# Kernel tuning notes

Measured on AMD Instinct MI355X. Metric: run time of the kernel, lower is better.

## Reference

```python
import jax, jax.numpy as jnp
import numpy as np

B, N, C, H, NRES = 32, 1024, 384, 1024, 20
NTAB = 21  # 20 aa + unknown, per AlphaFold residue_constants


def setup_inputs() -> dict:
    key = jax.random.key(0)
    ks = jax.random.split(key, 16)
    s = 0.02
    inp = {}
    inp['act'] = jax.random.normal(ks[0], (B, N, C), jnp.float32)
    inp['angles'] = jax.random.normal(ks[1], (B, N, 7, 2), jnp.float32)
    inp['rigids'] = jax.random.normal(ks[2], (B, N, 7), jnp.float32)
    inp['fixed_mask'] = jax.random.randint(ks[3], (B, N), 0, 2, jnp.int32)
    inp['seq_t'] = jax.random.randint(ks[4], (B, N), 0, NRES, jnp.int32)
    inp['residx_atom37_to_atom14'] = jax.random.randint(ks[5], (B, N, 37), 0, 14, jnp.int32)
    inp['ln_g'] = jnp.ones((C,), jnp.float32)
    inp['ln_b'] = jnp.zeros((C,), jnp.float32)
    inp['w1'] = jax.random.normal(ks[6], (C, H), jnp.float32) * s
    inp['b1'] = jnp.zeros((H,), jnp.float32)
    inp['w2'] = jax.random.normal(ks[7], (H, H), jnp.float32) * s
    inp['b2'] = jnp.zeros((H,), jnp.float32)
    inp['w3'] = jax.random.normal(ks[8], (H, NRES), jnp.float32) * s
    inp['b3'] = jnp.zeros((NRES,), jnp.float32)
    # stand-in residue_constants tables (same shapes/dtypes as AlphaFold's)
    inp['default_frames'] = jax.random.normal(ks[9], (NTAB, 8, 4, 4), jnp.float32)
    inp['group_idx'] = jax.random.randint(ks[10], (NTAB, 14), 0, 8, jnp.int32)
    inp['atom14_mask'] = (jax.random.uniform(ks[11], (NTAB, 14)) > 0.3).astype(jnp.float32)
    inp['atom37_mask'] = (jax.random.uniform(ks[12], (NTAB, 37)) > 0.3).astype(jnp.float32)
    inp['lit_positions'] = jax.random.normal(ks[13], (NTAB, 14, 3), jnp.float32)
    return inp


def quat_to_rot(q):
    q = q / jnp.sqrt(jnp.sum(q * q, axis=-1, keepdims=True) + 1e-8)
    w, x, y, z = q[..., 0], q[..., 1], q[..., 2], q[..., 3]
    r = jnp.stack([
        1 - 2 * (y * y + z * z), 2 * (x * y - w * z), 2 * (x * z + w * y),
        2 * (x * y + w * z), 1 - 2 * (x * x + z * z), 2 * (y * z - w * x),
        2 * (x * z - w * y), 2 * (y * z + w * x), 1 - 2 * (x * x + y * y)
    ], axis=-1)
    return r.reshape(q.shape[:-1] + (3, 3))


def compose(r1, t1, r2, t2):
    # rigid composition: (r1, t1) o (r2, t2)
    return (jnp.einsum('...ij,...jk->...ik', r1, r2),
            jnp.einsum('...ij,...j->...i', r1, t2) + t1)


def reference(act, angles, rigids, fixed_mask, seq_t, residx_atom37_to_atom14,
              ln_g, ln_b, w1, b1, w2, b2, w3, b3,
              default_frames, group_idx, atom14_mask, atom37_mask, lit_positions):
    # --- small MLP head ---
    mu = jnp.mean(act, axis=-1, keepdims=True)
    var = jnp.var(act, axis=-1, keepdims=True)
    h = (act - mu) / jnp.sqrt(var + 1e-5) * ln_g + ln_b
    h = jax.nn.relu(h @ w1 + b1)
    h = jax.nn.relu(h @ w2 + b2)
    logits = h @ w3 + b3                                # [B,N,20]
    p_0t = jax.nn.softmax(logits, axis=-1)
    seq0 = jnp.argmax(p_0t, axis=-1).astype(jnp.int32)
    seq0 = seq0 * (1 - fixed_mask) + seq_t * fixed_mask  # [B,N]

    # --- backbone frame from quaternion rigids ---
    rb = quat_to_rot(rigids[..., :4])                    # [B,N,3,3]
    tb = rigids[..., 4:]                                 # [B,N,3]

    # --- torsion_angles_to_frames ---
    df = default_frames[seq0]                            # [B,N,8,4,4]
    dr, dt = df[..., :3, :3], df[..., :3, 3]
    sin, cos = angles[..., 0], angles[..., 1]            # [B,N,7]
    z1 = jnp.zeros_like(sin[..., :1])
    sin8 = jnp.concatenate([z1, sin], axis=-1)           # backbone group has angle 0
    cos8 = jnp.concatenate([jnp.ones_like(z1), cos], axis=-1)
    zz, oo = jnp.zeros_like(sin8), jnp.ones_like(sin8)
    rx = jnp.stack([oo, zz, zz, zz, cos8, -sin8, zz, sin8, cos8], axis=-1)
    rx = rx.reshape(sin8.shape + (3, 3))                 # rotation about x-axis
    fr = jnp.einsum('bngij,bngjk->bngik', dr, rx)        # frames to backbone (pre-chain)
    ft = dt
    # chain chi2->chi1, chi3->chi2, chi4->chi3
    r5, t5 = compose(fr[..., 4, :, :], ft[..., 4, :], fr[..., 5, :, :], ft[..., 5, :])
    r6, t6 = compose(r5, t5, fr[..., 6, :, :], ft[..., 6, :])
    r7, t7 = compose(r6, t6, fr[..., 7, :, :], ft[..., 7, :])
    frot = jnp.concatenate([fr[..., :5, :, :], r5[..., None, :, :], r6[..., None, :, :], r7[..., None, :, :]], axis=-3)
    ftr = jnp.concatenate([ft[..., :5, :], t5[..., None, :], t6[..., None, :], t7[..., None, :]], axis=-2)
    grot, gtr = compose(rb[..., None, :, :], tb[..., None, :], frot, ftr)  # [B,N,8,3,3],[B,N,8,3]

    # --- frames_and_literature_positions_to_atom14_pos ---
    gi = group_idx[seq0]                                 # [B,N,14]
    ar = jnp.take_along_axis(grot, jnp.broadcast_to(gi[..., None, None], gi.shape + (3, 3)), axis=2)
    at = jnp.take_along_axis(gtr, jnp.broadcast_to(gi[..., None], gi.shape + (3,)), axis=2)
    lit = lit_positions[seq0]                            # [B,N,14,3]
    m14 = atom14_mask[seq0]                              # [B,N,14]
    pred = (jnp.einsum('bnaij,bnaj->bnai', ar, lit) + at) * m14[..., None]

    # --- atom14 -> atom37 gather ---
    idx = residx_atom37_to_atom14
    final = jnp.take_along_axis(pred, jnp.broadcast_to(idx[..., None], idx.shape + (3,)), axis=2)
    m37 = atom37_mask[seq0]                              # [B,N,37]
    return logits, seq0, pred, final, m14, m37
```

## Files before the change

kernel.cpp:

```cpp
#include <hip/hip_runtime.h>
#include <math.h>

#define B_ 32
#define N_ 1024
#define C_ 384
#define H_ 1024
#define NRES 20
#define NTAB 21
#define M_TOTAL (B_*N_)
#define BK 32

typedef __attribute__((ext_vector_type(8))) short bf16x8;
typedef __attribute__((ext_vector_type(4))) float f32x4;

#define GLOAD_LDS(gptr, lptr) \
    __builtin_amdgcn_global_load_lds( \
        (const __attribute__((address_space(1))) void*)(gptr), \
        (__attribute__((address_space(3))) void*)(lptr), 16, 0, 0)

__device__ inline short bf16_rne(float v) {
    unsigned u = __float_as_uint(v);
    unsigned r = u + 0x7fffu + ((u >> 16) & 1u);
    return (short)(r >> 16);
}
__device__ inline void split2(float v, short& h, short& l) {
    unsigned u = __float_as_uint(v);
    unsigned r = (u + 0x7fffu + ((u >> 16) & 1u)) & 0xffff0000u;
    h = (short)(r >> 16);
    l = bf16_rne(v - __uint_as_float(r));
}

__global__ __launch_bounds__(256) void ln_split_kernel(const float* __restrict__ act,
                                                       const float* __restrict__ lng,
                                                       const float* __restrict__ lnb,
                                                       short* __restrict__ Xh,
                                                       short* __restrict__ Xl) {
    int wave = threadIdx.x >> 6;
    int lane = threadIdx.x & 63;
    int row  = blockIdx.x * 4 + wave;
    const float* x = act + (size_t)row * C_;
    float v[6];
    float s = 0.f;
#pragma unroll
    for (int i = 0; i < 6; i++) { v[i] = x[lane + i*64]; s += v[i]; }
#pragma unroll
    for (int off = 32; off > 0; off >>= 1) s += __shfl_xor(s, off, 64);
    float mu = s * (1.0f/384.0f);
    float vs = 0.f;
#pragma unroll
    for (int i = 0; i < 6; i++) { float d = v[i]-mu; vs += d*d; }
#pragma unroll
    for (int off = 32; off > 0; off >>= 1) vs += __shfl_xor(vs, off, 64);
    float rstd = 1.0f / sqrtf(vs * (1.0f/384.0f) + 1e-5f);
#pragma unroll
    for (int i = 0; i < 6; i++) {
        int col = lane + i*64;
        float y = (v[i] - mu) * rstd * lng[col] + lnb[col];
        short h, l; split2(y, h, l);
        Xh[(size_t)row * C_ + col] = h;
        Xl[(size_t)row * C_ + col] = l;
    }
}

__global__ __launch_bounds__(256) void conv_w_kernel(const float* __restrict__ w,
                                                     short* __restrict__ th,
                                                     short* __restrict__ tl,
                                                     int K, int N, int Npad) {
    __shared__ float t[32][33];
    int n0 = blockIdx.x * 32, k0 = blockIdx.y * 32;
    int tx = threadIdx.x & 31, ty = threadIdx.x >> 5;
#pragma unroll
    for (int i = ty; i < 32; i += 8) {
        int k = k0 + i, n = n0 + tx;
        t[i][tx] = (n < N) ? w[(size_t)k * N + n] : 0.f;
    }
    __syncthreads();
#pragma unroll
    for (int i = ty; i < 32; i += 8) {
        int n = n0 + i, k = k0 + tx;
        short h, l; split2(t[tx][i], h, l);
        th[(size_t)n * K + k] = h;
        tl[(size_t)n * K + k] = l;
    }
}

__global__ __launch_bounds__(512, 2) void presplit_gemm256(
    const short* __restrict__ Ahg, const short* __restrict__ Alg,
    const short* __restrict__ BTh, const short* __restrict__ BTl,
    const float* __restrict__ bias,
    short* __restrict__ Ch, short* __restrict__ Cl,
    int K, int ldc)
{
    __shared__ short P[4][2][256][32];
    const int BUFS = 256*32;
    int tid = threadIdx.x;
    int m0 = blockIdx.x * 256;
    int n0 = blockIdx.y * 256;
    int lane = tid & 63, wv = tid >> 6;
    int wr = wv >> 2, wc = wv & 3;
    int fm = lane & 15, kg = lane >> 4;

    int pl = wv >> 1, hf = wv & 1;
    const short* gsrc = (pl == 0) ? Ahg : (pl == 1) ? Alg : (pl == 2) ? BTh : BTl;
    int base = (pl < 2) ? m0 : n0;
    int swcb = (lane & 3) ^ ((lane >> 3) & 3);
    const short* gp = gsrc + (size_t)(base + hf*128 + (lane >> 2)) * K + swcb * 8;
    short* lpl = &P[pl][0][0][0] + hf * (128*32);

    int sz = (kg ^ ((fm >> 1) & 3)) * 8;
    const short* raH = &P[0][0][wr*128 + fm][0] + sz;
    const short* raL = &P[1][0][wr*128 + fm][0] + sz;
    const short* rbH = &P[2][0][wc*64  + fm][0] + sz;
    const short* rbL = &P[3][0][wc*64  + fm][0] + sz;

#define STAGE8(bsel, koff) \
    { _Pragma("unroll") \
      for (int c = 0; c < 8; c++) \
          GLOAD_LDS(gp + (size_t)(c*16) * K + (koff), lpl + (bsel)*BUFS + c*512); }

#define TRIPLE(ai, aj, AH, AL, BH, BL) { \
    f32x4 cc = acc[ai][aj]; \
    cc = __builtin_amdgcn_mfma_f32_16x16x32_bf16(AL, BH, cc, 0, 0, 0); \
    cc = __builtin_amdgcn_mfma_f32_16x16x32_bf16(AH, BL, cc, 0, 0, 0); \
    cc = __builtin_amdgcn_mfma_f32_16x16x32_bf16(AH, BH, cc, 0, 0, 0); \
    acc[ai][aj] = cc; }

    f32x4 acc[8][4] = {};
    const int NT = K / BK;

    bf16x8 aAh[4], aAl[4], aBh[4], aBl[4];
    bf16x8 bAh[2], bAl[2], bBh[2], bBl[2];

    STAGE8(0, 0);
    asm volatile("s_waitcnt vmcnt(0)" ::: "memory");
    __builtin_amdgcn_s_barrier();
#pragma unroll
    for (int i = 0; i < 4; i++) {
        aAh[i] = *(const bf16x8*)(raH + i*512);
        aAl[i] = *(const bf16x8*)(raL + i*512);
    }

    for (int t = 0; t < NT; ++t) {
        int cur = t & 1, nxt = cur ^ 1;
        size_t koff = (size_t)(t + 1) * BK;
        bool pf = (t + 1 < NT);

#pragma unroll
        for (int j = 0; j < 2; j++) {
            bAh[j] = *(const bf16x8*)(rbH + cur*BUFS + j*512);
            bAl[j] = *(const bf16x8*)(rbL + cur*BUFS + j*512);
            bBh[j] = *(const bf16x8*)(rbH + cur*BUFS + (2+j)*512);
            bBl[j] = *(const bf16x8*)(rbL + cur*BUFS + (2+j)*512);
        }
        if (pf) STAGE8(nxt, koff);
        __builtin_amdgcn_s_setprio(1);
#pragma unroll
        for (int i = 0; i < 4; i++)
#pragma unroll
            for (int j = 0; j < 2; j++) TRIPLE(i, j, aAh[i], aAl[i], bAh[j], bAl[j]);
        __builtin_amdgcn_s_setprio(0);
        __builtin_amdgcn_s_barrier();

#pragma unroll
        for (int i = 0; i < 4; i++) {
            aBh[i] = *(const bf16x8*)(raH + cur*BUFS + (4+i)*512);
            aBl[i] = *(const bf16x8*)(raL + cur*BUFS + (4+i)*512);
        }
        __builtin_amdgcn_s_setprio(1);
#pragma unroll
        for (int i = 0; i < 4; i++)
#pragma unroll
            for (int j = 0; j < 2; j++) TRIPLE(i, 2+j, aAh[i], aAl[i], bBh[j], bBl[j]);
        __builtin_amdgcn_s_setprio(0);
        __builtin_amdgcn_s_barrier();

        __builtin_amdgcn_s_setprio(1);
#pragma unroll
        for (int i = 0; i < 4; i++)
#pragma unroll
            for (int j = 0; j < 2; j++) TRIPLE(4+i, 2+j, aBh[i], aBl[i], bBh[j], bBl[j]);
        __builtin_amdgcn_s_setprio(0);
        asm volatile("s_waitcnt vmcnt(0)" ::: "memory");
        __builtin_amdgcn_s_barrier();

        if (pf) {
#pragma unroll
            for (int i = 0; i < 4; i++) {
                aAh[i] = *(const bf16x8*)(raH + nxt*BUFS + i*512);
                aAl[i] = *(const bf16x8*)(raL + nxt*BUFS + i*512);
            }
        }
        __builtin_amdgcn_s_setprio(1);
#pragma unroll
        for (int i = 0; i < 4; i++)
#pragma unroll
            for (int j = 0; j < 2; j++) TRIPLE(4+i, j, aBh[i], aBl[i], bAh[j], bAl[j]);
        __builtin_amdgcn_s_setprio(0);
        __builtin_amdgcn_s_barrier();
    }

#pragma unroll
    for (int i = 0; i < 8; i++)
#pragma unroll
        for (int j = 0; j < 4; j++) {
            int col = n0 + wc*64 + j*16 + fm;
            float bs = bias[col];
#pragma unroll
            for (int r = 0; r < 4; r++) {
                int row = m0 + wr*128 + i*16 + kg*4 + r;
                float v = fmaxf(acc[i][j][r] + bs, 0.f);
                short h, l; split2(v, h, l);
                Ch[(size_t)row * ldc + col] = h;
                Cl[(size_t)row * ldc + col] = l;
            }
        }
#undef STAGE8
#undef TRIPLE
}

__global__ __launch_bounds__(256) void gemm3_fused(
    const short* __restrict__ Ahg, const short* __restrict__ Alg,
    const short* __restrict__ BTh, const short* __restrict__ BTl,
    const float* __restrict__ b3,
    const int* __restrict__ fixed_mask, const int* __restrict__ seq_t,
    float* __restrict__ out_logits, float* __restrict__ seq_out,
    int* __restrict__ seq_int, int m0c)
{
    __shared__ short Ah[2][64][32], Al[2][64][32];
    __shared__ short Bh[2][32][32], Bl[2][32][32];
    __shared__ float slog[64][33];
    int tid = threadIdx.x;
    int m0 = blockIdx.x * 64;
    int lane = tid & 63, wv = tid >> 6;
    int wm = wv * 16;
    int fm = lane & 15, kg = lane >> 4;

    const short* gsrc = (wv == 0) ? Ahg : (wv == 1) ? Alg : (wv == 2) ? BTh : BTl;
    short* lb0 = (wv == 0) ? &Ah[0][0][0] : (wv == 1) ? &Al[0][0][0]
               : (wv == 2) ? &Bh[0][0][0] : &Bl[0][0][0];
    int pstride = (wv < 2) ? (64*32) : (32*32);
    int ncalls  = (wv < 2) ? 4 : 2;
    int base = (wv < 2) ? m0 : 0;
    int swcb = (lane & 3) ^ ((lane >> 3) & 3);
    const short* gp = gsrc + (size_t)(base + (lane >> 2)) * H_ + swcb * 8;

    int saz = (kg ^ (((wm + fm) >> 1) & 3)) * 8;
    int sbz[2];
#pragma unroll
    for (int j = 0; j < 2; j++) sbz[j] = (kg ^ (((j*16 + fm) >> 1) & 3)) * 8;

    f32x4 acc[2] = {};
    const int NT = H_ / BK;

    for (int c = 0; c < ncalls; c++)
        GLOAD_LDS(gp + (size_t)(c * 16) * H_, lb0 + c * 512);

    for (int t = 0; t < NT; ++t) {
        __syncthreads();

        if (t + 1 < NT) {
            short* lb = lb0 + ((t + 1) & 1) * pstride;
            size_t k0n = (size_t)(t + 1) * BK;
            for (int c = 0; c < ncalls; c++)
                GLOAD_LDS(gp + (size_t)(c * 16) * H_ + k0n, lb + c * 512);
        }

        int cur = t & 1;
        bf16x8 a_h = *(bf16x8*)&Ah[cur][wm + fm][saz];
        bf16x8 a_l = *(bf16x8*)&Al[cur][wm + fm][saz];
        bf16x8 b_h[2], b_l[2];
#pragma unroll
        for (int j = 0; j < 2; j++) {
            b_h[j] = *(bf16x8*)&Bh[cur][j*16 + fm][sbz[j]];
            b_l[j] = *(bf16x8*)&Bl[cur][j*16 + fm][sbz[j]];
        }
#pragma unroll
        for (int j = 0; j < 2; j++) {
            f32x4 c = acc[j];
            c = __builtin_amdgcn_mfma_f32_16x16x32_bf16(a_l, b_h[j], c, 0, 0, 0);
            c = __builtin_amdgcn_mfma_f32_16x16x32_bf16(a_h, b_l[j], c, 0, 0, 0);
            c = __builtin_amdgcn_mfma_f32_16x16x32_bf16(a_h, b_h[j], c, 0, 0, 0);
            acc[j] = c;
        }
    }

#pragma unroll
    for (int j = 0; j < 2; j++)
#pragma unroll
        for (int r = 0; r < 4; r++)
            slog[wm + kg*4 + r][j*16 + fm] = acc[j][r];
    __syncthreads();

    if (tid < 64) {
        int grow = m0c + m0 + tid;
        float best = -1e30f; int bi = 0;
        float* lg = out_logits + (size_t)grow * NRES;
#pragma unroll
        for (int n = 0; n < NRES; n++) {
            float s = slog[tid][n] + b3[n];
            lg[n] = s;
            if (s > best) { best = s; bi = n; }
        }
        int fmk = fixed_mask[grow];
        int s = fmk ? seq_t[grow] : bi;
        seq_int[grow] = s;
        seq_out[grow] = (float)s;
    }
}

__global__ __launch_bounds__(128) void geom_kernel(
    const float* __restrict__ angles, const float* __restrict__ rigids,
    const int* __restrict__ seq0i, const int* __restrict__ residx,
    const float* __restrict__ dframes, const int* __restrict__ gidx,
    const float* __restrict__ a14m, const float* __restrict__ a37m,
    const float* __restrict__ litp,
    float* __restrict__ out_pred, float* __restrict__ out_final,
    float* __restrict__ out_m14, float* __restrict__ out_m37)
{
    __shared__ float sdf[NTAB*8*16];
    __shared__ int   sgi[NTAB*14];
    __shared__ float sm14[NTAB*14];
    __shared__ float sm37[NTAB*37];
    __shared__ float slit[NTAB*14*3];
    __shared__ float predL[128][43];

    for (int i = threadIdx.x; i < NTAB*128; i += 128) sdf[i] = dframes[i];
    for (int i = threadIdx.x; i < NTAB*14; i += 128) { sgi[i] = gidx[i]; sm14[i] = a14m[i]; }
    for (int i = threadIdx.x; i < NTAB*37; i += 128) sm37[i] = a37m[i];
    for (int i = threadIdx.x; i < NTAB*42; i += 128) slit[i] = litp[i];
    __syncthreads();

    int p = blockIdx.x * 128 + threadIdx.x;
    int s = seq0i[p];

    const float* rg = rigids + (size_t)p * 7;
    float qw = rg[0], qx = rg[1], qy = rg[2], qz = rg[3];
    float tbx = rg[4], tby = rg[5], tbz = rg[6];
    float qn = 1.0f / sqrtf(qw*qw + qx*qx + qy*qy + qz*qz + 1e-8f);
    qw *= qn; qx *= qn; qy *= qn; qz *= qn;
    float rb[9];
    rb[0] = 1.f - 2.f*(qy*qy + qz*qz); rb[1] = 2.f*(qx*qy - qw*qz); rb[2] = 2.f*(qx*qz + qw*qy);
    rb[3] = 2.f*(qx*qy + qw*qz); rb[4] = 1.f - 2.f*(qx*qx + qz*qz); rb[5] = 2.f*(qy*qz - qw*qx);
    rb[6] = 2.f*(qx*qz - qw*qy); rb[7] = 2.f*(qy*qz + qw*qx); rb[8] = 1.f - 2.f*(qx*qx + qy*qy);

    float fr[8][9], ft[8][3];
    const float* ang = angles + (size_t)p * 14;
#pragma unroll
    for (int g = 0; g < 8; g++) {
        const float* df = &sdf[(s*8 + g)*16];
        float c, sn;
        if (g == 0) { c = 1.f; sn = 0.f; }
        else { sn = ang[(g-1)*2 + 0]; c = ang[(g-1)*2 + 1]; }
#pragma unroll
        for (int i = 0; i < 3; i++) {
            float d0 = df[i*4+0], d1 = df[i*4+1], d2 = df[i*4+2];
            fr[g][i*3+0] = d0;
            fr[g][i*3+1] = d1*c + d2*sn;
            fr[g][i*3+2] = d2*c - d1*sn;
            ft[g][i] = df[i*4+3];
        }
    }
#pragma unroll
    for (int g = 5; g <= 7; g++) {
        float r[9], t[3];
        const float* r1 = fr[g-1];
        const float* t1 = ft[g-1];
#pragma unroll
        for (int i = 0; i < 3; i++) {
#pragma unroll
            for (int j = 0; j < 3; j++)
                r[i*3+j] = r1[i*3+0]*fr[g][0*3+j] + r1[i*3+1]*fr[g][1*3+j] + r1[i*3+2]*fr[g][2*3+j];
            t[i] = r1[i*3+0]*ft[g][0] + r1[i*3+1]*ft[g][1] + r1[i*3+2]*ft[g][2] + t1[i];
        }
#pragma unroll
        for (int i = 0; i < 9; i++) fr[g][i] = r[i];
#pragma unroll
        for (int i = 0; i < 3; i++) ft[g][i] = t[i];
    }
#pragma unroll
    for (int g = 0; g < 8; g++) {
        float r[9], t[3];
#pragma unroll
        for (int i = 0; i < 3; i++) {
#pragma unroll
            for (int j = 0; j < 3; j++)
                r[i*3+j] = rb[i*3+0]*fr[g][0*3+j] + rb[i*3+1]*fr[g][1*3+j] + rb[i*3+2]*fr[g][2*3+j];
            t[i] = rb[i*3+0]*ft[g][0] + rb[i*3+1]*ft[g][1] + rb[i*3+2]*ft[g][2];
        }
#pragma unroll
        for (int i = 0; i < 9; i++) fr[g][i] = r[i];
        ft[g][0]=t[0]+tbx; ft[g][1]=t[1]+tby; ft[g][2]=t[2]+tbz;
    }
#pragma unroll
    for (int g = 0; g < 8; g++) {
#pragma unroll
        for (int a = 0; a < 14; a++) {
            if (sgi[s*14 + a] == g) {
                float m  = sm14[s*14 + a];
                float lx = slit[(s*14 + a)*3 + 0];
                float ly = slit[(s*14 + a)*3 + 1];
                float lz = slit[(s*14 + a)*3 + 2];
                float px = (fr[g][0]*lx + fr[g][1]*ly + fr[g][2]*lz + ft[g][0]) * m;
                float py = (fr[g][3]*lx + fr[g][4]*ly + fr[g][5]*lz + ft[g][1]) * m;
                float pz = (fr[g][6]*lx + fr[g][7]*ly + fr[g][8]*lz + ft[g][2]) * m;
                predL[threadIdx.x][a*3+0] = px;
                predL[threadIdx.x][a*3+1] = py;
                predL[threadIdx.x][a*3+2] = pz;
                out_pred[((size_t)p*14 + a)*3 + 0] = px;
                out_pred[((size_t)p*14 + a)*3 + 1] = py;
                out_pred[((size_t)p*14 + a)*3 + 2] = pz;
            }
        }
    }
#pragma unroll
    for (int a = 0; a < 14; a++) out_m14[(size_t)p*14 + a] = sm14[s*14 + a];

    const int* idx = residx + (size_t)p * 37;
#pragma unroll
    for (int a = 0; a < 37; a++) {
        int id = idx[a];
        out_final[((size_t)p*37 + a)*3 + 0] = predL[threadIdx.x][id*3+0];
        out_final[((size_t)p*37 + a)*3 + 1] = predL[threadIdx.x][id*3+1];
        out_final[((size_t)p*37 + a)*3 + 2] = predL[threadIdx.x][id*3+2];
        out_m37[(size_t)p*37 + a] = sm37[s*37 + a];
    }
}

extern "C" void kernel_launch(void* const* d_in, const int* in_sizes, int n_in,
                              void* d_out, int out_size, void* d_ws, size_t ws_size,
                              hipStream_t stream) {
    const float* act        = (const float*)d_in[0];
    const float* angles     = (const float*)d_in[1];
    const float* rigids     = (const float*)d_in[2];
    const int*   fixed_mask = (const int*)d_in[3];
    const int*   seq_t      = (const int*)d_in[4];
    const int*   residx     = (const int*)d_in[5];
    const float* lng        = (const float*)d_in[6];
    const float* lnb        = (const float*)d_in[7];
    const float* w1         = (const float*)d_in[8];
    const float* b1         = (const float*)d_in[9];
    const float* w2         = (const float*)d_in[10];
    const float* b2         = (const float*)d_in[11];
    const float* w3         = (const float*)d_in[12];
    const float* b3         = (const float*)d_in[13];
    const float* dfr        = (const float*)d_in[14];
    const int*   gidx       = (const int*)d_in[15];
    const float* a14m       = (const float*)d_in[16];
    const float* a37m       = (const float*)d_in[17];
    const float* litp       = (const float*)d_in[18];

    float* out        = (float*)d_out;
    float* out_logits = out;
    float* out_seq    = out_logits + (size_t)M_TOTAL * NRES;
    float* out_pred   = out_seq    + (size_t)M_TOTAL;
    float* out_final  = out_pred   + (size_t)M_TOTAL * 42;
    float* out_m14    = out_final  + (size_t)M_TOTAL * 111;
    float* out_m37    = out_m14    + (size_t)M_TOTAL * 14;

    char* wsp = (char*)d_ws;
    int*   seq0i = (int*)wsp;   wsp += (size_t)M_TOTAL * sizeof(int);
    short* w1h   = (short*)wsp; wsp += (size_t)H_ * C_ * sizeof(short);
    short* w1l   = (short*)wsp; wsp += (size_t)H_ * C_ * sizeof(short);
    short* w2h   = (short*)wsp; wsp += (size_t)H_ * H_ * sizeof(short);
    short* w2l   = (short*)wsp; wsp += (size_t)H_ * H_ * sizeof(short);
    short* w3h   = (short*)wsp; wsp += (size_t)128 * H_ * sizeof(short);
    short* w3l   = (short*)wsp; wsp += (size_t)128 * H_ * sizeof(short);
    short* Xh    = (short*)wsp; wsp += (size_t)M_TOTAL * C_ * sizeof(short);
    short* Xl    = (short*)wsp; wsp += (size_t)M_TOTAL * C_ * sizeof(short);

    size_t fixed_bytes = (size_t)(wsp - (char*)d_ws);
    size_t per_row = 4ull * H_ * sizeof(short);
    size_t avail = ws_size - fixed_bytes;
    int chunkM = 4096;
    if (avail >= (size_t)M_TOTAL * per_row)      chunkM = M_TOTAL;
    else if (avail >= 16384ull * per_row)        chunkM = 16384;
    else if (avail >= 8192ull * per_row)         chunkM = 8192;

    short* H1h = (short*)wsp; wsp += (size_t)chunkM * H_ * sizeof(short);
    short* H1l = (short*)wsp; wsp += (size_t)chunkM * H_ * sizeof(short);
    short* H2h = (short*)wsp; wsp += (size_t)chunkM * H_ * sizeof(short);
    short* H2l = (short*)wsp;

    conv_w_kernel<<<dim3(H_/32, C_/32), 256, 0, stream>>>(w1, w1h, w1l, C_, H_, H_);
    conv_w_kernel<<<dim3(H_/32, H_/32), 256, 0, stream>>>(w2, w2h, w2l, H_, H_, H_);
    conv_w_kernel<<<dim3(128/32, H_/32), 256, 0, stream>>>(w3, w3h, w3l, H_, NRES, 128);

    ln_split_kernel<<<M_TOTAL/4, 256, 0, stream>>>(act, lng, lnb, Xh, Xl);

    for (int c = 0; c < M_TOTAL / chunkM; c++) {
        int m0 = c * chunkM;
        presplit_gemm256<<<dim3(chunkM/256, H_/256), 512, 0, stream>>>(
            Xh + (size_t)m0 * C_, Xl + (size_t)m0 * C_, w1h, w1l, b1, H1h, H1l, C_, H_);
        presplit_gemm256<<<dim3(chunkM/256, H_/256), 512, 0, stream>>>(
            H1h, H1l, w2h, w2l, b2, H2h, H2l, H_, H_);
        gemm3_fused<<<chunkM/64, 256, 0, stream>>>(H2h, H2l, w3h, w3l, b3,
                                                   fixed_mask, seq_t,
                                                   out_logits, out_seq, seq0i, m0);
    }

    geom_kernel<<<M_TOTAL/128, 128, 0, stream>>>(angles, rigids, seq0i, residx,
                                                 dfr, gidx, a14m, a37m, litp,
                                                 out_pred, out_final, out_m14, out_m37);
}
```

Measured before the change: 475.5 us.

## Use 32x32x16 MFMA in main GEMMs and split-K the final logits GEMM

The 256x256 split-bf16 GEMM now uses 32x32x16 MFMA instructions with 16-float accumulators instead of 16x16x32, changing fragment loads, LDS addressing and the epilogue row mapping. The aim is fewer instructions and less LDS read traffic per FLOP. The small third GEMM is split into four K-slices written to a scratch buffer that aliases H1, then reduced by a new kernel that adds the bias and does the argmax. This exposes more parallelism for that thin GEMM at the cost of an extra launch and extra partial-sum traffic.

```diff
diff --git a/kernel.cpp b/kernel.cpp
--- a/kernel.cpp
+++ b/kernel.cpp
@@ -9,9 +9,11 @@
 #define NTAB 21
 #define M_TOTAL (B_*N_)
 #define BK 32
+#define KS 4
 
 typedef __attribute__((ext_vector_type(8))) short bf16x8;
 typedef __attribute__((ext_vector_type(4))) float f32x4;
+typedef __attribute__((ext_vector_type(16))) float f32x16;
 
 #define GLOAD_LDS(gptr, lptr) \
     __builtin_amdgcn_global_load_lds( \
@@ -98,7 +100,7 @@
     int n0 = blockIdx.y * 256;
     int lane = tid & 63, wv = tid >> 6;
     int wr = wv >> 2, wc = wv & 3;
-    int fm = lane & 15, kg = lane >> 4;
+    int r5 = lane & 31, q5 = lane >> 5;
 
     int pl = wv >> 1, hf = wv & 1;
     const short* gsrc = (pl == 0) ? Ahg : (pl == 1) ? Alg : (pl == 2) ? BTh : BTl;
@@ -107,37 +109,46 @@
     const short* gp = gsrc + (size_t)(base + hf*128 + (lane >> 2)) * K + swcb * 8;
     short* lpl = &P[pl][0][0][0] + hf * (128*32);
 
-    int sz = (kg ^ ((fm >> 1) & 3)) * 8;
-    const short* raH = &P[0][0][wr*128 + fm][0] + sz;
-    const short* raL = &P[1][0][wr*128 + fm][0] + sz;
-    const short* rbH = &P[2][0][wc*64  + fm][0] + sz;
-    const short* rbL = &P[3][0][wc*64  + fm][0] + sz;
+    int szl = (r5 >> 1) & 3;
+    int cbA[2] = { (q5 ^ szl) * 8, ((2 + q5) ^ szl) * 8 };
+    const short* pA0 = &P[0][0][wr*128 + r5][0];
+    const short* pA1 = &P[1][0][wr*128 + r5][0];
+    const short* pB0 = &P[2][0][wc*64  + r5][0];
+    const short* pB1 = &P[3][0][wc*64  + r5][0];
 
 #define STAGE8(bsel, koff) \
     { _Pragma("unroll") \
       for (int c = 0; c < 8; c++) \
           GLOAD_LDS(gp + (size_t)(c*16) * K + (koff), lpl + (bsel)*BUFS + c*512); }
 
-#define TRIPLE(ai, aj, AH, AL, BH, BL) { \
-    f32x4 cc = acc[ai][aj]; \
-    cc = __builtin_amdgcn_mfma_f32_16x16x32_bf16(AL, BH, cc, 0, 0, 0); \
-    cc = __builtin_amdgcn_mfma_f32_16x16x32_bf16(AH, BL, cc, 0, 0, 0); \
-    cc = __builtin_amdgcn_mfma_f32_16x16x32_bf16(AH, BH, cc, 0, 0, 0); \
-    acc[ai][aj] = cc; }
-
-    f32x4 acc[8][4] = {};
+#define TRIPLE32(ci, cj, AH, AL, BH, BL) { \
+    f32x16 cc = acc[ci][cj]; \
+    cc = __builtin_amdgcn_mfma_f32_32x32x16_bf16(AL, BH, cc, 0, 0, 0); \
+    cc = __builtin_amdgcn_mfma_f32_32x32x16_bf16(AH, BL, cc, 0, 0, 0); \
+    cc = __builtin_amdgcn_mfma_f32_32x32x16_bf16(AH, BH, cc, 0, 0, 0); \
+    acc[ci][cj] = cc; }
+
+    f32x16 acc[4][2] = {};
     const int NT = K / BK;
 
-    bf16x8 aAh[4], aAl[4], aBh[4], aBl[4];
+    bf16x8 aAh[2][2], aAl[2][2], aBh[2][2], aBl[2][2];
     bf16x8 bAh[2], bAl[2], bBh[2], bBl[2];
 
     STAGE8(0, 0);
     asm volatile("s_waitcnt vmcnt(0)" ::: "memory");
     __builtin_amdgcn_s_barrier();
-#pragma unroll
-    for (int i = 0; i < 4; i++) {
-        aAh[i] = *(const bf16x8*)(raH + i*512);
-        aAl[i] = *(const bf16x8*)(raL + i*512);
+    __builtin_amdgcn_sched_barrier(0);
+#pragma unroll
+    for (int i2 = 0; i2 < 2; i2++)
+#pragma unroll
+        for (int s = 0; s < 2; s++) {
+            aAh[i2][s] = *(const bf16x8*)(pA0 + i2*1024 + cbA[s]);
+            aAl[i2][s] = *(const bf16x8*)(pA1 + i2*1024 + cbA[s]);
+        }
+#pragma unroll
+    for (int s = 0; s < 2; s++) {
+        bAh[s] = *(const bf16x8*)(pB0 + cbA[s]);
+        bAl[s] = *(const bf16x8*)(pB1 + cbA[s]);
     }
 
     for (int t = 0; t < NT; ++t) {
@@ -145,92 +156,101 @@
         size_t koff = (size_t)(t + 1) * BK;
         bool pf = (t + 1 < NT);
 
-#pragma unroll
-        for (int j = 0; j < 2; j++) {
-            bAh[j] = *(const bf16x8*)(rbH + cur*BUFS + j*512);
-            bAl[j] = *(const bf16x8*)(rbL + cur*BUFS + j*512);
-            bBh[j] = *(const bf16x8*)(rbH + cur*BUFS + (2+j)*512);
-            bBl[j] = *(const bf16x8*)(rbL + cur*BUFS + (2+j)*512);
-        }
         if (pf) STAGE8(nxt, koff);
+#pragma unroll
+        for (int s = 0; s < 2; s++) {
+            bBh[s] = *(const bf16x8*)(pB0 + cur*BUFS + 1024 + cbA[s]);
+            bBl[s] = *(const bf16x8*)(pB1 + cur*BUFS + 1024 + cbA[s]);
+        }
         __builtin_amdgcn_s_setprio(1);
 #pragma unroll
-        for (int i = 0; i < 4; i++)
-#pragma unroll
-            for (int j = 0; j < 2; j++) TRIPLE(i, j, aAh[i], aAl[i], bAh[j], bAl[j]);
+        for (int i2 = 0; i2 < 2; i2++)
+#pragma unroll
+            for (int s = 0; s < 2; s++)
+                TRIPLE32(i2, 0, aAh[i2][s], aAl[i2][s], bAh[s], bAl[s]);
         __builtin_amdgcn_s_setprio(0);
         __builtin_amdgcn_s_barrier();
 
 #pragma unroll
-        for (int i = 0; i < 4; i++) {
-            aBh[i] = *(const bf16x8*)(raH + cur*BUFS + (4+i)*512);
-            aBl[i] = *(const bf16x8*)(raL + cur*BUFS + (4+i)*512);
-        }
+        for (int i2 = 0; i2 < 2; i2++)
+#pragma unroll
+            for (int s = 0; s < 2; s++) {
+                aBh[i2][s] = *(const bf16x8*)(pA0 + cur*BUFS + (2+i2)*1024 + cbA[s]);
+                aBl[i2][s] = *(const bf16x8*)(pA1 + cur*BUFS + (2+i2)*1024 + cbA[s]);
+            }
         __builtin_amdgcn_s_setprio(1);
 #pragma unroll
-        for (int i = 0; i < 4; i++)
-#pragma unroll
-            for (int j = 0; j < 2; j++) TRIPLE(i, 2+j, aAh[i], aAl[i], bBh[j], bBl[j]);
+        for (int i2 = 0; i2 < 2; i2++)
+#pragma unroll
+            for (int s = 0; s < 2; s++)
+                TRIPLE32(i2, 1, aAh[i2][s], aAl[i2][s], bBh[s], bBl[s]);
         __builtin_amdgcn_s_setprio(0);
         __builtin_amdgcn_s_barrier();
 
         __builtin_amdgcn_s_setprio(1);
 #pragma unroll
-        for (int i = 0; i < 4; i++)
-#pragma unroll
-            for (int j = 0; j < 2; j++) TRIPLE(4+i, 2+j, aBh[i], aBl[i], bBh[j], bBl[j]);
+        for (int i2 = 0; i2 < 2; i2++)
+#pragma unroll
+            for (int s = 0; s < 2; s++)
+                TRIPLE32(2+i2, 0, aBh[i2][s], aBl[i2][s], bAh[s], bAl[s]);
         __builtin_amdgcn_s_setprio(0);
         asm volatile("s_waitcnt vmcnt(0)" ::: "memory");
         __builtin_amdgcn_s_barrier();
+        __builtin_amdgcn_sched_barrier(0);
 
         if (pf) {
 #pragma unroll
-            for (int i = 0; i < 4; i++) {
-                aAh[i] = *(const bf16x8*)(raH + nxt*BUFS + i*512);
-                aAl[i] = *(const bf16x8*)(raL + nxt*BUFS + i*512);
+            for (int i2 = 0; i2 < 2; i2++)
+#pragma unroll
+                for (int s = 0; s < 2; s++) {
+                    aAh[i2][s] = *(const bf16x8*)(pA0 + nxt*BUFS + i2*1024 + cbA[s]);
+                    aAl[i2][s] = *(const bf16x8*)(pA1 + nxt*BUFS + i2*1024 + cbA[s]);
+                }
+#pragma unroll
+            for (int s = 0; s < 2; s++) {
+                bAh[s] = *(const bf16x8*)(pB0 + nxt*BUFS + cbA[s]);
+                bAl[s] = *(const bf16x8*)(pB1 + nxt*BUFS + cbA[s]);
             }
         }
         __builtin_amdgcn_s_setprio(1);
 #pragma unroll
-        for (int i = 0; i < 4; i++)
-#pragma unroll
-            for (int j = 0; j < 2; j++) TRIPLE(4+i, j, aBh[i], aBl[i], bAh[j], bAl[j]);
+        for (int i2 = 0; i2 < 2; i2++)
+#pragma unroll
+            for (int s = 0; s < 2; s++)
+                TRIPLE32(2+i2, 1, aBh[i2][s], aBl[i2][s], bBh[s], bBl[s]);
         __builtin_amdgcn_s_setprio(0);
         __builtin_amdgcn_s_barrier();
     }
 
 #pragma unroll
-    for (int i = 0; i < 8; i++)
-#pragma unroll
-        for (int j = 0; j < 4; j++) {
-            int col = n0 + wc*64 + j*16 + fm;
+    for (int i = 0; i < 4; i++)
+#pragma unroll
+        for (int j = 0; j < 2; j++) {
+            int col = n0 + wc*64 + j*32 + r5;
             float bs = bias[col];
 #pragma unroll
-            for (int r = 0; r < 4; r++) {
-                int row = m0 + wr*128 + i*16 + kg*4 + r;
-                float v = fmaxf(acc[i][j][r] + bs, 0.f);
+            for (int g = 0; g < 16; g++) {
+                int row = m0 + wr*128 + i*32 + (g & 3) + 8*(g >> 2) + 4*q5;
+                float v = fmaxf(acc[i][j][g] + bs, 0.f);
                 short h, l; split2(v, h, l);
                 Ch[(size_t)row * ldc + col] = h;
                 Cl[(size_t)row * ldc + col] = l;
             }
         }
 #undef STAGE8
-#undef TRIPLE
-}
-
-__global__ __launch_bounds__(256) void gemm3_fused(
+#undef TRIPLE32
+}
+
+__global__ __launch_bounds__(256) void gemm3_partial(
     const short* __restrict__ Ahg, const short* __restrict__ Alg,
     const short* __restrict__ BTh, const short* __restrict__ BTl,
-    const float* __restrict__ b3,
-    const int* __restrict__ fixed_mask, const int* __restrict__ seq_t,
-    float* __restrict__ out_logits, float* __restrict__ seq_out,
-    int* __restrict__ seq_int, int m0c)
+    float* __restrict__ Pbuf, int chunkM)
 {
     __shared__ short Ah[2][64][32], Al[2][64][32];
     __shared__ short Bh[2][32][32], Bl[2][32][32];
-    __shared__ float slog[64][33];
     int tid = threadIdx.x;
     int m0 = blockIdx.x * 64;
+    int ks = blockIdx.y;
     int lane = tid & 63, wv = tid >> 6;
     int wm = wv * 16;
     int fm = lane & 15, kg = lane >> 4;
@@ -242,7 +262,7 @@
     int ncalls  = (wv < 2) ? 4 : 2;
     int base = (wv < 2) ? m0 : 0;
     int swcb = (lane & 3) ^ ((lane >> 3) & 3);
-    const short* gp = gsrc + (size_t)(base + (lane >> 2)) * H_ + swcb * 8;
+    const short* gp = gsrc + (size_t)(base + (lane >> 2)) * H_ + ks * (H_/KS) + swcb * 8;
 
     int saz = (kg ^ (((wm + fm) >> 1) & 3)) * 8;
     int sbz[2];
@@ -250,7 +270,7 @@
     for (int j = 0; j < 2; j++) sbz[j] = (kg ^ (((j*16 + fm) >> 1) & 3)) * 8;
 
     f32x4 acc[2] = {};
-    const int NT = H_ / BK;
+    const int NT = (H_/KS) / BK;
 
     for (int c = 0; c < ncalls; c++)
         GLOAD_LDS(gp + (size_t)(c * 16) * H_, lb0 + c * 512);
@@ -288,24 +308,32 @@
     for (int j = 0; j < 2; j++)
 #pragma unroll
         for (int r = 0; r < 4; r++)
-            slog[wm + kg*4 + r][j*16 + fm] = acc[j][r];
-    __syncthreads();
-
-    if (tid < 64) {
-        int grow = m0c + m0 + tid;
-        float best = -1e30f; int bi = 0;
-        float* lg = out_logits + (size_t)grow * NRES;
-#pragma unroll
-        for (int n = 0; n < NRES; n++) {
-            float s = slog[tid][n] + b3[n];
-            lg[n] = s;
-            if (s > best) { best = s; bi = n; }
-        }
-        int fmk = fixed_mask[grow];
-        int s = fmk ? seq_t[grow] : bi;
-        seq_int[grow] = s;
-        seq_out[grow] = (float)s;
-    }
+            Pbuf[((size_t)ks * chunkM + m0 + wm + kg*4 + r) * 32 + j*16 + fm] = acc[j][r];
+}
+
+__global__ __launch_bounds__(256) void logits_reduce(
+    const float* __restrict__ Pbuf, const float* __restrict__ b3,
+    const int* __restrict__ fixed_mask, const int* __restrict__ seq_t,
+    float* __restrict__ out_logits, float* __restrict__ seq_out,
+    int* __restrict__ seq_int, int chunkM, int m0c)
+{
+    int lrow = blockIdx.x * 256 + threadIdx.x;
+    int grow = m0c + lrow;
+    float best = -1e30f; int bi = 0;
+    float* lg = out_logits + (size_t)grow * NRES;
+#pragma unroll
+    for (int n = 0; n < NRES; n++) {
+        float s = b3[n];
+#pragma unroll
+        for (int k = 0; k < KS; k++)
+            s += Pbuf[((size_t)k * chunkM + lrow) * 32 + n];
+        lg[n] = s;
+        if (s > best) { best = s; bi = n; }
+    }
+    int fmk = fixed_mask[grow];
+    int sv = fmk ? seq_t[grow] : bi;
+    seq_int[grow] = sv;
+    seq_out[grow] = (float)sv;
 }
 
 __global__ __launch_bounds__(128) void geom_kernel(
@@ -481,6 +509,8 @@
     short* H2h = (short*)wsp; wsp += (size_t)chunkM * H_ * sizeof(short);
     short* H2l = (short*)wsp;
 
+    float* Pbuf = (float*)H1h;
+
     conv_w_kernel<<<dim3(H_/32, C_/32), 256, 0, stream>>>(w1, w1h, w1l, C_, H_, H_);
     conv_w_kernel<<<dim3(H_/32, H_/32), 256, 0, stream>>>(w2, w2h, w2l, H_, H_, H_);
     conv_w_kernel<<<dim3(128/32, H_/32), 256, 0, stream>>>(w3, w3h, w3l, H_, NRES, 128);
@@ -493,9 +523,10 @@
             Xh + (size_t)m0 * C_, Xl + (size_t)m0 * C_, w1h, w1l, b1, H1h, H1l, C_, H_);
         presplit_gemm256<<<dim3(chunkM/256, H_/256), 512, 0, stream>>>(
             H1h, H1l, w2h, w2l, b2, H2h, H2l, H_, H_);
-        gemm3_fused<<<chunkM/64, 256, 0, stream>>>(H2h, H2l, w3h, w3l, b3,
-                                                   fixed_mask, seq_t,
-                                                   out_logits, out_seq, seq0i, m0);
+        gemm3_partial<<<dim3(chunkM/64, KS), 256, 0, stream>>>(
+            H2h, H2l, w3h, w3l, Pbuf, chunkM);
+        logits_reduce<<<chunkM/256, 256, 0, stream>>>(
+            Pbuf, b3, fixed_mask, seq_t, out_logits, out_seq, seq0i, chunkM, m0);
     }
 
     geom_kernel<<<M_TOTAL/128, 128, 0, stream>>>(angles, rigids, seq0i, residx,
```

Result: slower. 499.0 us (+4.9%).

## Split-K the final logits GEMM and re-pipeline LDS fragment loads in main GEMM

Applied to the files above, without the earlier changes.

The third GEMM (H→20 logits) is split four ways along K with a grid y-dimension, and each split writes partials into a scratch buffer that reuses the H1 workspace. A separate reduce kernel sums the partials, adds the bias, takes the argmax and applies the fixed mask. This raises the block count for the skinny GEMM, at the cost of an extra launch and a round trip through global memory. The main 256-tile GEMM loop is also unrolled by two with static buffer indices, and its LDS fragment loads are spread across the MFMA phases with sched_barriers, so that more loads overlap with compute.

```diff
diff --git a/kernel.cpp b/kernel.cpp
--- a/kernel.cpp
+++ b/kernel.cpp
@@ -9,6 +9,7 @@
 #define NTAB 21
 #define M_TOTAL (B_*N_)
 #define BK 32
+#define KS 4
 
 typedef __attribute__((ext_vector_type(8))) short bf16x8;
 typedef __attribute__((ext_vector_type(4))) float f32x4;
@@ -134,70 +135,90 @@
     STAGE8(0, 0);
     asm volatile("s_waitcnt vmcnt(0)" ::: "memory");
     __builtin_amdgcn_s_barrier();
+    __builtin_amdgcn_sched_barrier(0);
 #pragma unroll
     for (int i = 0; i < 4; i++) {
         aAh[i] = *(const bf16x8*)(raH + i*512);
         aAl[i] = *(const bf16x8*)(raL + i*512);
     }
-
-    for (int t = 0; t < NT; ++t) {
-        int cur = t & 1, nxt = cur ^ 1;
-        size_t koff = (size_t)(t + 1) * BK;
-        bool pf = (t + 1 < NT);
-
-#pragma unroll
-        for (int j = 0; j < 2; j++) {
-            bAh[j] = *(const bf16x8*)(rbH + cur*BUFS + j*512);
-            bAl[j] = *(const bf16x8*)(rbL + cur*BUFS + j*512);
-            bBh[j] = *(const bf16x8*)(rbH + cur*BUFS + (2+j)*512);
-            bBl[j] = *(const bf16x8*)(rbL + cur*BUFS + (2+j)*512);
-        }
-        if (pf) STAGE8(nxt, koff);
-        __builtin_amdgcn_s_setprio(1);
-#pragma unroll
-        for (int i = 0; i < 4; i++)
-#pragma unroll
-            for (int j = 0; j < 2; j++) TRIPLE(i, j, aAh[i], aAl[i], bAh[j], bAl[j]);
-        __builtin_amdgcn_s_setprio(0);
-        __builtin_amdgcn_s_barrier();
-
-#pragma unroll
-        for (int i = 0; i < 4; i++) {
-            aBh[i] = *(const bf16x8*)(raH + cur*BUFS + (4+i)*512);
-            aBl[i] = *(const bf16x8*)(raL + cur*BUFS + (4+i)*512);
-        }
-        __builtin_amdgcn_s_setprio(1);
-#pragma unroll
-        for (int i = 0; i < 4; i++)
-#pragma unroll
-            for (int j = 0; j < 2; j++) TRIPLE(i, 2+j, aAh[i], aAl[i], bBh[j], bBl[j]);
-        __builtin_amdgcn_s_setprio(0);
-        __builtin_amdgcn_s_barrier();
-
-        __builtin_amdgcn_s_setprio(1);
-#pragma unroll
-        for (int i = 0; i < 4; i++)
-#pragma unroll
-            for (int j = 0; j < 2; j++) TRIPLE(4+i, 2+j, aBh[i], aBl[i], bBh[j], bBl[j]);
-        __builtin_amdgcn_s_setprio(0);
-        asm volatile("s_waitcnt vmcnt(0)" ::: "memory");
-        __builtin_amdgcn_s_barrier();
-
-        if (pf) {
-#pragma unroll
-            for (int i = 0; i < 4; i++) {
-                aAh[i] = *(const bf16x8*)(raH + nxt*BUFS + i*512);
-                aAl[i] = *(const bf16x8*)(raL + nxt*BUFS + i*512);
-            }
-        }
-        __builtin_amdgcn_s_setprio(1);
-#pragma unroll
-        for (int i = 0; i < 4; i++)
-#pragma unroll
-            for (int j = 0; j < 2; j++) TRIPLE(4+i, j, aBh[i], aBl[i], bAh[j], bAl[j]);
-        __builtin_amdgcn_s_setprio(0);
-        __builtin_amdgcn_s_barrier();
-    }
+#pragma unroll
+    for (int j = 0; j < 2; j++) {
+        bAh[j] = *(const bf16x8*)(rbH + j*512);
+        bAl[j] = *(const bf16x8*)(rbL + j*512);
+    }
+
+#define STEP(CUR, NXT, T) { \
+    const bool pf = (T) + 1 < NT; \
+    const size_t koff = (size_t)((T) + 1) * BK; \
+     \
+    if (pf) STAGE8(NXT, koff); \
+    bBh[0] = *(const bf16x8*)(rbH + (CUR)*BUFS + 2*512); \
+    bBl[0] = *(const bf16x8*)(rbL + (CUR)*BUFS + 2*512); \
+    bBh[1] = *(const bf16x8*)(rbH + (CUR)*BUFS + 3*512); \
+    bBl[1] = *(const bf16x8*)(rbL + (CUR)*BUFS + 3*512); \
+    aBh[0] = *(const bf16x8*)(raH + (CUR)*BUFS + 4*512); \
+    aBl[0] = *(const bf16x8*)(raL + (CUR)*BUFS + 4*512); \
+    __builtin_amdgcn_s_setprio(1); \
+    _Pragma("unroll") \
+    for (int i = 0; i < 4; i++) \
+        _Pragma("unroll") \
+        for (int j = 0; j < 2; j++) TRIPLE(i, j, aAh[i], aAl[i], bAh[j], bAl[j]); \
+    __builtin_amdgcn_s_setprio(0); \
+    __builtin_amdgcn_s_barrier(); \
+     \
+    _Pragma("unroll") \
+    for (int i = 1; i < 4; i++) { \
+        aBh[i] = *(const bf16x8*)(raH + (CUR)*BUFS + (4+i)*512); \
+        aBl[i] = *(const bf16x8*)(raL + (CUR)*BUFS + (4+i)*512); \
+    } \
+    __builtin_amdgcn_s_setprio(1); \
+    _Pragma("unroll") \
+    for (int i = 0; i < 4; i++) \
+        _Pragma("unroll") \
+        for (int j = 0; j < 2; j++) TRIPLE(i, 2+j, aAh[i], aAl[i], bBh[j], bBl[j]); \
+    __builtin_amdgcn_s_setprio(0); \
+    asm volatile("s_waitcnt vmcnt(0)" ::: "memory"); \
+    __builtin_amdgcn_s_barrier(); \
+    __builtin_amdgcn_sched_barrier(0); \
+     \
+    if (pf) { \
+        _Pragma("unroll") \
+        for (int i = 0; i < 3; i++) { \
+            aAh[i] = *(const bf16x8*)(raH + (NXT)*BUFS + i*512); \
+            aAl[i] = *(const bf16x8*)(raL + (NXT)*BUFS + i*512); \
+        } \
+    } \
+    __builtin_amdgcn_s_setprio(1); \
+    _Pragma("unroll") \
+    for (int i = 0; i < 4; i++) \
+        _Pragma("unroll") \
+        for (int j = 0; j < 2; j++) TRIPLE(4+i, j, aBh[i], aBl[i], bAh[j], bAl[j]); \
+    __builtin_amdgcn_s_setprio(0); \
+    __builtin_amdgcn_s_barrier(); \
+     \
+    if (pf) { \
+        aAh[3] = *(const bf16x8*)(raH + (NXT)*BUFS + 3*512); \
+        aAl[3] = *(const bf16x8*)(raL + (NXT)*BUFS + 3*512); \
+        _Pragma("unroll") \
+        for (int j = 0; j < 2; j++) { \
+            bAh[j] = *(const bf16x8*)(rbH + (NXT)*BUFS + j*512); \
+            bAl[j] = *(const bf16x8*)(rbL + (NXT)*BUFS + j*512); \
+        } \
+    } \
+    __builtin_amdgcn_s_setprio(1); \
+    _Pragma("unroll") \
+    for (int i = 0; i < 4; i++) \
+        _Pragma("unroll") \
+        for (int j = 0; j < 2; j++) TRIPLE(4+i, 2+j, aBh[i], aBl[i], bBh[j], bBl[j]); \
+    __builtin_amdgcn_s_setprio(0); \
+    __builtin_amdgcn_s_barrier(); \
+}
+
+    for (int t = 0; t < NT; t += 2) {
+        STEP(0, 1, t);
+        STEP(1, 0, t + 1);
+    }
+#undef STEP
 
 #pragma unroll
     for (int i = 0; i < 8; i++)
@@ -218,19 +239,16 @@
 #undef TRIPLE
 }
 
-__global__ __launch_bounds__(256) void gemm3_fused(
+__global__ __launch_bounds__(256) void gemm3_partial(
     const short* __restrict__ Ahg, const short* __restrict__ Alg,
     const short* __restrict__ BTh, const short* __restrict__ BTl,
-    const float* __restrict__ b3,
-    const int* __restrict__ fixed_mask, const int* __restrict__ seq_t,
-    float* __restrict__ out_logits, float* __restrict__ seq_out,
-    int* __restrict__ seq_int, int m0c)
+    float* __restrict__ Pbuf, int chunkM)
 {
     __shared__ short Ah[2][64][32], Al[2][64][32];
     __shared__ short Bh[2][32][32], Bl[2][32][32];
-    __shared__ float slog[64][33];
     int tid = threadIdx.x;
     int m0 = blockIdx.x * 64;
+    int ks = blockIdx.y;
     int lane = tid & 63, wv = tid >> 6;
     int wm = wv * 16;
     int fm = lane & 15, kg = lane >> 4;
@@ -242,7 +260,7 @@
     int ncalls  = (wv < 2) ? 4 : 2;
     int base = (wv < 2) ? m0 : 0;
     int swcb = (lane & 3) ^ ((lane >> 3) & 3);
-    const short* gp = gsrc + (size_t)(base + (lane >> 2)) * H_ + swcb * 8;
+    const short* gp = gsrc + (size_t)(base + (lane >> 2)) * H_ + ks * (H_/KS) + swcb * 8;
 
     int saz = (kg ^ (((wm + fm) >> 1) & 3)) * 8;
     int sbz[2];
@@ -250,7 +268,7 @@
     for (int j = 0; j < 2; j++) sbz[j] = (kg ^ (((j*16 + fm) >> 1) & 3)) * 8;
 
     f32x4 acc[2] = {};
-    const int NT = H_ / BK;
+    const int NT = (H_/KS) / BK;
 
     for (int c = 0; c < ncalls; c++)
         GLOAD_LDS(gp + (size_t)(c * 16) * H_, lb0 + c * 512);
@@ -288,24 +306,32 @@
     for (int j = 0; j < 2; j++)
 #pragma unroll
         for (int r = 0; r < 4; r++)
-            slog[wm + kg*4 + r][j*16 + fm] = acc[j][r];
-    __syncthreads();
-
-    if (tid < 64) {
-        int grow = m0c + m0 + tid;
-        float best = -1e30f; int bi = 0;
-        float* lg = out_logits + (size_t)grow * NRES;
-#pragma unroll
-        for (int n = 0; n < NRES; n++) {
-            float s = slog[tid][n] + b3[n];
-            lg[n] = s;
-            if (s > best) { best = s; bi = n; }
-        }
-        int fmk = fixed_mask[grow];
-        int s = fmk ? seq_t[grow] : bi;
-        seq_int[grow] = s;
-        seq_out[grow] = (float)s;
-    }
+            Pbuf[((size_t)ks * chunkM + m0 + wm + kg*4 + r) * 32 + j*16 + fm] = acc[j][r];
+}
+
+__global__ __launch_bounds__(256) void logits_reduce(
+    const float* __restrict__ Pbuf, const float* __restrict__ b3,
+    const int* __restrict__ fixed_mask, const int* __restrict__ seq_t,
+    float* __restrict__ out_logits, float* __restrict__ seq_out,
+    int* __restrict__ seq_int, int chunkM, int m0c)
+{
+    int lrow = blockIdx.x * 256 + threadIdx.x;
+    int grow = m0c + lrow;
+    float best = -1e30f; int bi = 0;
+    float* lg = out_logits + (size_t)grow * NRES;
+#pragma unroll
+    for (int n = 0; n < NRES; n++) {
+        float s = b3[n];
+#pragma unroll
+        for (int k = 0; k < KS; k++)
+            s += Pbuf[((size_t)k * chunkM + lrow) * 32 + n];
+        lg[n] = s;
+        if (s > best) { best = s; bi = n; }
+    }
+    int fmk = fixed_mask[grow];
+    int sv = fmk ? seq_t[grow] : bi;
+    seq_int[grow] = sv;
+    seq_out[grow] = (float)sv;
 }
 
 __global__ __launch_bounds__(128) void geom_kernel(
@@ -481,6 +507,8 @@
     short* H2h = (short*)wsp; wsp += (size_t)chunkM * H_ * sizeof(short);
     short* H2l = (short*)wsp;
 
+    float* Pbuf = (float*)H1h;
+
     conv_w_kernel<<<dim3(H_/32, C_/32), 256, 0, stream>>>(w1, w1h, w1l, C_, H_, H_);
     conv_w_kernel<<<dim3(H_/32, H_/32), 256, 0, stream>>>(w2, w2h, w2l, H_, H_, H_);
     conv_w_kernel<<<dim3(128/32, H_/32), 256, 0, stream>>>(w3, w3h, w3l, H_, NRES, 128);
@@ -493,9 +521,10 @@
             Xh + (size_t)m0 * C_, Xl + (size_t)m0 * C_, w1h, w1l, b1, H1h, H1l, C_, H_);
         presplit_gemm256<<<dim3(chunkM/256, H_/256), 512, 0, stream>>>(
             H1h, H1l, w2h, w2l, b2, H2h, H2l, H_, H_);
-        gemm3_fused<<<chunkM/64, 256, 0, stream>>>(H2h, H2l, w3h, w3l, b3,
-                                                   fixed_mask, seq_t,
-                                                   out_logits, out_seq, seq0i, m0);
+        gemm3_partial<<<dim3(chunkM/64, KS), 256, 0, stream>>>(
+            H2h, H2l, w3h, w3l, Pbuf, chunkM);
+        logits_reduce<<<chunkM/256, 256, 0, stream>>>(
+            Pbuf, b3, fixed_mask, seq_t, out_logits, out_seq, seq0i, chunkM, m0);
     }
 
     geom_kernel<<<M_TOTAL/128, 128, 0, stream>>>(angles, rigids, seq0i, residx,
```

New measurement: 562.0 us. +18.2%, slower.
